# Performance work log

Hardware: AMD Instinct MI355X
Metric: run time of the kernel (lower is better)

Reference implementation:

```python
import jax, jax.numpy as jnp
import numpy as np

N_EMBD = 1024
N_HEAD = 16
HEAD_DIM = N_EMBD // N_HEAD
NEG = -1e9


def setup_inputs() -> dict:
    key = jax.random.key(0)
    ks = jax.random.split(key, 5)
    B, S = 2, 2048
    x = jax.random.normal(ks[0], (B, S, N_EMBD), dtype=jnp.float32)
    # qkv_proj: Linear(n_embd, 3*n_embd) -> weight used as x @ W_qkv (W stored [in, out])
    scale = 1.0 / np.sqrt(N_EMBD)
    W_qkv = jax.random.normal(ks[1], (N_EMBD, 3 * N_EMBD), dtype=jnp.float32) * scale
    b_qkv = jax.random.normal(ks[2], (3 * N_EMBD,), dtype=jnp.float32) * 0.02
    W_out = jax.random.normal(ks[3], (N_EMBD, N_EMBD), dtype=jnp.float32) * scale
    b_out = jax.random.normal(ks[4], (N_EMBD,), dtype=jnp.float32) * 0.02
    return {"x": x, "W_qkv": W_qkv, "b_qkv": b_qkv, "W_out": W_out, "b_out": b_out}


def reference(x, W_qkv, b_qkv, W_out, b_out):
    B, S, E = x.shape
    qkv = x @ W_qkv + b_qkv                      # [B,S,3E]
    q, k, v = jnp.split(qkv, 3, axis=-1)
    # [B,S,E] -> [B,H,S,D]
    def split_heads(t):
        return t.reshape(B, S, N_HEAD, HEAD_DIM).transpose(0, 2, 1, 3)
    q, k, v = split_heads(q), split_heads(k), split_heads(v)
    scores = jnp.einsum("bhqd,bhkd->bhqk", q, k) / jnp.sqrt(jnp.float32(HEAD_DIM))
    causal = jnp.tril(jnp.ones((S, S), dtype=bool))
    scores = jnp.where(causal, scores, NEG)
    attn = jax.nn.softmax(scores, axis=-1)
    out = jnp.einsum("bhqk,bhkd->bhqd", attn, v)  # [B,H,S,D]
    out = out.transpose(0, 2, 1, 3).reshape(B, S, E)
    return out @ W_out + b_out
```

## Files before the change

### kernel.cpp

```cpp
#include <hip/hip_runtime.h>
#include <hip/hip_bf16.h>

#define BATCH 2
#define SEQ   2048
#define EMBD  1024
#define NHEAD 16
#define HDIM  64
#define QKV3  (3 * EMBD)

#define QSCALE 0.18033688011112042f
#define SCLAMP 86.56f

typedef __attribute__((ext_vector_type(8))) __bf16 bf16x8;
typedef __attribute__((ext_vector_type(4))) __bf16 bf16x4;
typedef __attribute__((ext_vector_type(4))) float f32x4;

__device__ __forceinline__ float fast_exp2(float x) {
#if __has_builtin(__builtin_amdgcn_exp2f)
    return __builtin_amdgcn_exp2f(x);
#else
    return exp2f(x);
#endif
}

__global__ __launch_bounds__(256) void cast_f32_bf16(
    const float* __restrict__ in, __bf16* __restrict__ out)
{
    int i = (blockIdx.x * 256 + threadIdx.x) * 8;
    float4 a = *(const float4*)&in[i];
    float4 b = *(const float4*)&in[i + 4];
    bf16x8 o;
    o[0] = (__bf16)a.x; o[1] = (__bf16)a.y; o[2] = (__bf16)a.z; o[3] = (__bf16)a.w;
    o[4] = (__bf16)b.x; o[5] = (__bf16)b.y; o[6] = (__bf16)b.z; o[7] = (__bf16)b.w;
    *(bf16x8*)&out[i] = o;
}

__global__ __launch_bounds__(256) void transpose_cast_bf16(
    const float* __restrict__ in, __bf16* __restrict__ out, int K, int N)
{
    __shared__ float t[64][65];
    const int k0 = blockIdx.y * 64, n0 = blockIdx.x * 64;
    const int tid = threadIdx.x;
    #pragma unroll
    for (int p = 0; p < 4; p++) {
        int kr = p * 16 + (tid >> 4);
        int c4 = (tid & 15) * 4;
        float4 v = *(const float4*)&in[(size_t)(k0 + kr) * N + n0 + c4];
        t[kr][c4] = v.x; t[kr][c4 + 1] = v.y; t[kr][c4 + 2] = v.z; t[kr][c4 + 3] = v.w;
    }
    __syncthreads();
    #pragma unroll
    for (int p = 0; p < 4; p++) {
        int nr = p * 16 + (tid >> 4);
        int k4 = (tid & 15) * 4;
        bf16x4 o;
        o[0] = (__bf16)t[k4 + 0][nr];
        o[1] = (__bf16)t[k4 + 1][nr];
        o[2] = (__bf16)t[k4 + 2][nr];
        o[3] = (__bf16)t[k4 + 3][nr];
        *(bf16x4*)&out[(size_t)(n0 + nr) * K + k0 + k4] = o;
    }
}

__global__ __launch_bounds__(256) void transpose_v_bf16(
    const __bf16* __restrict__ qkv, __bf16* __restrict__ vt)
{
    __shared__ __bf16 t[64][72];
    const int k0 = blockIdx.x * 64;
    const int bh = blockIdx.y;
    const int b = bh >> 4, h = bh & 15;
    const size_t base = (size_t)b * SEQ * QKV3 + 2 * EMBD + h * HDIM;
    const int tid = threadIdx.x;
    #pragma unroll
    for (int it = 0; it < 2; it++) {
        int flat = it * 256 + tid;
        int kr = flat >> 3;
        int d0 = (flat & 7) * 8;
        bf16x8 v = *(const bf16x8*)&qkv[base + (size_t)(k0 + kr) * QKV3 + d0];
        #pragma unroll
        for (int i = 0; i < 8; i++) t[kr][d0 + i] = v[i];
    }
    __syncthreads();
    #pragma unroll
    for (int it = 0; it < 2; it++) {
        int flat = it * 256 + tid;
        int d  = flat >> 3;
        int kc = (flat & 7) * 8;
        bf16x8 o;
        #pragma unroll
        for (int i = 0; i < 8; i++) o[i] = t[kc + i][d];
        *(bf16x8*)&vt[((size_t)bh * 64 + d) * SEQ + k0 + kc] = o;
    }
}

template<bool OUT_BF16>
__global__ __launch_bounds__(256) void gemm_bt_mfma(
    const __bf16* __restrict__ A,
    const __bf16* __restrict__ Bt,
    const float* __restrict__ bias,
    void* __restrict__ Cv,
    int M, int N, int K, int nscale)
{
    __shared__ __align__(16) __bf16 As[128 * 32];
    __shared__ __align__(16) __bf16 Bs[128 * 32];

    const int tid  = threadIdx.x;
    const int lane = tid & 63;
    const int wave = tid >> 6;
    const int wm = (wave >> 1) * 64;
    const int wn = (wave & 1) * 64;
    const int m0 = blockIdx.y * 128;
    const int n0 = blockIdx.x * 128;
    const int lm = lane & 15;
    const int kq = lane >> 4;

    f32x4 acc[4][4] = {};

    for (int k0 = 0; k0 < K; k0 += 32) {
        __syncthreads();
        #pragma unroll
        for (int r = 0; r < 2; r++) {
            int flat = r * 256 + tid;
            int row  = flat >> 2;
            int off  = (flat & 3) * 16;
            const char* ga = (const char*)(A + (size_t)(m0 + row) * K + k0) + off;
            char* la = (char*)As + flat * 16;
            __builtin_amdgcn_global_load_lds(
                (const __attribute__((address_space(1))) void*)ga,
                (__attribute__((address_space(3))) void*)la, 16, 0, 0);
            const char* gb = (const char*)(Bt + (size_t)(n0 + row) * K + k0) + off;
            char* lb = (char*)Bs + flat * 16;
            __builtin_amdgcn_global_load_lds(
                (const __attribute__((address_space(1))) void*)gb,
                (__attribute__((address_space(3))) void*)lb, 16, 0, 0);
        }
        __syncthreads();

        bf16x8 af[4], bf[4];
        #pragma unroll
        for (int t = 0; t < 4; t++) {
            af[t] = *(const bf16x8*)&As[(wm + t * 16 + lm) * 32 + kq * 8];
            bf[t] = *(const bf16x8*)&Bs[(wn + t * 16 + lm) * 32 + kq * 8];
        }
        #pragma unroll
        for (int i = 0; i < 4; i++)
            #pragma unroll
            for (int j = 0; j < 4; j++)
                acc[i][j] = __builtin_amdgcn_mfma_f32_16x16x32_bf16(
                    af[i], bf[j], acc[i][j], 0, 0, 0);
    }

    const int r0 = kq * 4;
    #pragma unroll
    for (int i = 0; i < 4; i++) {
        #pragma unroll
        for (int j = 0; j < 4; j++) {
            int col = n0 + wn + j * 16 + lm;
            float bv = bias[col];
            float sc = (col < nscale) ? QSCALE : 1.0f;
            #pragma unroll
            for (int r = 0; r < 4; r++) {
                int row = m0 + wm + i * 16 + r0 + r;
                float val = (acc[i][j][r] + bv) * sc;
                if (OUT_BF16) ((__bf16*)Cv)[(size_t)row * N + col] = (__bf16)val;
                else          ((float*)Cv)[(size_t)row * N + col] = val;
            }
        }
    }
}

__global__ __launch_bounds__(256) void attn_kpar_mfma(
    const __bf16* __restrict__ qkv, const __bf16* __restrict__ vt,
    __bf16* __restrict__ attn)
{
    __shared__ __align__(16) char smem[34304];

    const int tid  = threadIdx.x;
    const int wave = tid >> 6;
    const int lane = tid & 63;
    const int quad = lane >> 4;
    const int c    = lane & 15;

    const int bh = blockIdx.x;
    const int b  = bh >> 4;
    const int h  = bh & 15;
    const int qblk = (int)(gridDim.y - 1) - blockIdx.y;
    const int q0 = qblk * 64;

    const size_t base = (size_t)b * SEQ * QKV3;
    const int hoff = h * HDIM;
    const __bf16* vbase = vt + (size_t)bh * 64 * SEQ;

    bf16x8 aq[4][2];
    #pragma unroll
    for (int qf = 0; qf < 4; qf++) {
        const __bf16* qrow = qkv + base +
            (size_t)(q0 + qf * 16 + c) * QKV3 + hoff + quad * 8;
        aq[qf][0] = *(const bf16x8*)(qrow);
        aq[qf][1] = *(const bf16x8*)(qrow + 32);
    }

    f32x4 acc[4][4] = {};
    float lpart[4] = {};

    char* pbw = smem + wave * 8192;
    const int ntiles = qblk + 1;

    for (int t = wave; t < ntiles; t += 4) {
        const int k0 = t * 64;
        const bool diag = (t == ntiles - 1);

        #pragma unroll
        for (int jj = 0; jj < 4; jj++) {
            const __bf16* krow = qkv + base +
                (size_t)(k0 + jj * 16 + c) * QKV3 + EMBD + hoff + quad * 8;
            bf16x8 bk0 = *(const bf16x8*)(krow);
            bf16x8 bk1 = *(const bf16x8*)(krow + 32);
            const int kb = k0 + jj * 16 + quad * 4;
            const int wb = (jj >> 1) * 1024 + (((jj & 1) * 2 + (quad >> 1))) * 256
                         + c * 16 + (quad & 1) * 8;
            #pragma unroll
            for (int qf = 0; qf < 4; qf++) {
                f32x4 s = {};
                s = __builtin_amdgcn_mfma_f32_16x16x32_bf16(bk0, aq[qf][0], s, 0, 0, 0);
                s = __builtin_amdgcn_mfma_f32_16x16x32_bf16(bk1, aq[qf][1], s, 0, 0, 0);
                const int qa = q0 + qf * 16 + c;
                bf16x4 pk;
                #pragma unroll
                for (int r = 0; r < 4; r++) {
                    float p;
                    if (diag && (kb + r > qa)) p = 0.f;
                    else p = fast_exp2(fminf(s[r], SCLAMP));
                    lpart[qf] += p;
                    pk[r] = (__bf16)p;
                }
                *(bf16x4*)(pbw + qf * 2048 + wb) = pk;
            }
        }

        __builtin_amdgcn_s_setprio(1);
        #pragma unroll
        for (int kc = 0; kc < 2; kc++) {
            bf16x8 ap[4];
            #pragma unroll
            for (int qf = 0; qf < 4; qf++)
                ap[qf] = *(const bf16x8*)(pbw + qf * 2048 + kc * 1024 + lane * 16);
            #pragma unroll
            for (int dd = 0; dd < 4; dd++) {
                const __bf16* vr = vbase + (size_t)(dd * 16 + c) * SEQ
                                 + k0 + kc * 32 + quad * 8;
                bf16x8 bv = *(const bf16x8*)(vr);
                #pragma unroll
                for (int qf = 0; qf < 4; qf++)
                    acc[qf][dd] = __builtin_amdgcn_mfma_f32_16x16x32_bf16(
                        ap[qf], bv, acc[qf][dd], 0, 0, 0);
            }
        }
        __builtin_amdgcn_s_setprio(0);
    }

    #pragma unroll
    for (int qf = 0; qf < 4; qf++) {
        float v = lpart[qf];
        v += __shfl_xor(v, 16);
        v += __shfl_xor(v, 32);
        lpart[qf] = v;
    }

    __syncthreads();

    float* Ored = (float*)smem;
    float* lred = (float*)(smem + 33792);

    if (wave < 2) {
        float* R = Ored + wave * (64 * 66);
        #pragma unroll
        for (int qf = 0; qf < 4; qf++) {
            #pragma unroll
            for (int dd = 0; dd < 4; dd++)
                #pragma unroll
                for (int r = 0; r < 4; r++)
                    R[(qf * 16 + quad * 4 + r) * 66 + dd * 16 + c] = acc[qf][dd][r];
            if (quad == 0) lred[wave * 64 + qf * 16 + c] = lpart[qf];
        }
    }
    __syncthreads();
    if (wave >= 2) {
        float* R = Ored + (wave - 2) * (64 * 66);
        #pragma unroll
        for (int qf = 0; qf < 4; qf++) {
            #pragma unroll
            for (int dd = 0; dd < 4; dd++)
                #pragma unroll
                for (int r = 0; r < 4; r++)
                    R[(qf * 16 + quad * 4 + r) * 66 + dd * 16 + c] += acc[qf][dd][r];
            if (quad == 0) lred[(wave - 2) * 64 + qf * 16 + c] += lpart[qf];
        }
    }
    __syncthreads();

    #pragma unroll
    for (int it = 0; it < 2; it++) {
        const int flat = it * 256 + tid;
        const int row = flat >> 3;
        const int cg  = flat & 7;
        const float l = lred[row] + lred[64 + row];
        const float inv = 1.f / l;
        const float* R0 = Ored + row * 66 + cg * 8;
        const float* R1 = R0 + 64 * 66;
        bf16x8 o;
        #pragma unroll
        for (int i = 0; i < 8; i++) o[i] = (__bf16)((R0[i] + R1[i]) * inv);
        *(bf16x8*)&attn[((size_t)b * SEQ + q0 + row) * EMBD + hoff + cg * 8] = o;
    }
}

extern "C" void kernel_launch(void* const* d_in, const int* in_sizes, int n_in,
                              void* d_out, int out_size, void* d_ws, size_t ws_size,
                              hipStream_t stream)
{
    const float* x     = (const float*)d_in[0];
    const float* W_qkv = (const float*)d_in[1];
    const float* b_qkv = (const float*)d_in[2];
    const float* W_out = (const float*)d_in[3];
    const float* b_out = (const float*)d_in[4];
    float* out = (float*)d_out;

    const int M = BATCH * SEQ;

    __bf16* xbf    = (__bf16*)d_ws;
    __bf16* Wqkv_t = xbf    + (size_t)M * EMBD;
    __bf16* Wout_t = Wqkv_t + (size_t)QKV3 * EMBD;
    __bf16* qkv    = Wout_t + (size_t)EMBD * EMBD;
    __bf16* attn   = qkv    + (size_t)M * QKV3;
    __bf16* vtbuf  = attn   + (size_t)M * EMBD;

    cast_f32_bf16<<<(M * EMBD) / (256 * 8), 256, 0, stream>>>(x, xbf);
    {
        dim3 g(QKV3 / 64, EMBD / 64);
        transpose_cast_bf16<<<g, 256, 0, stream>>>(W_qkv, Wqkv_t, EMBD, QKV3);
    }
    {
        dim3 g(EMBD / 64, EMBD / 64);
        transpose_cast_bf16<<<g, 256, 0, stream>>>(W_out, Wout_t, EMBD, EMBD);
    }
    {
        dim3 grid(QKV3 / 128, M / 128);
        gemm_bt_mfma<true><<<grid, 256, 0, stream>>>(xbf, Wqkv_t, b_qkv, qkv, M, QKV3, EMBD, EMBD);
    }
    {
        dim3 grid(SEQ / 64, BATCH * NHEAD);
        transpose_v_bf16<<<grid, 256, 0, stream>>>(qkv, vtbuf);
    }
    {
        dim3 grid(BATCH * NHEAD, SEQ / 64);
        attn_kpar_mfma<<<grid, 256, 0, stream>>>(qkv, vtbuf, attn);
    }
    {
        dim3 grid(EMBD / 128, M / 128);
        gemm_bt_mfma<false><<<grid, 256, 0, stream>>>(attn, Wout_t, b_out, out, M, EMBD, EMBD, 0);
    }
}
```

Baseline: 203.7 us.

## Prefetch K tiles into registers and remap blocks across XCDs

Each wave now loads the K tile for its next iteration into registers during the current iteration, and issues the V loads at the start of the tile so their latency overlaps the QK^T and softmax work. The block index is also remapped so consecutive hardware blocks, which are spread round-robin over the 8 XCDs, land on the same head's query blocks per XCD to improve L2 reuse of K/V. The change raises register pressure, which may lower occupancy, and the remap assumes a fixed grid of 1024 blocks.

```diff
diff --git a/kernel.cpp b/kernel.cpp
--- a/kernel.cpp
+++ b/kernel.cpp
@@ -181,10 +181,12 @@
     const int quad = lane >> 4;
     const int c    = lane & 15;
 
-    const int bh = blockIdx.x;
+    const int hw = (int)(blockIdx.x + gridDim.x * blockIdx.y);
+    const int logical = (hw & 7) * 128 + (hw >> 3);
+    const int bh   = logical >> 5;
+    const int qblk = 31 - (logical & 31);
     const int b  = bh >> 4;
     const int h  = bh & 15;
-    const int qblk = (int)(gridDim.y - 1) - blockIdx.y;
     const int q0 = qblk * 64;
 
     const size_t base = (size_t)b * SEQ * QKV3;
@@ -206,24 +208,40 @@
     char* pbw = smem + wave * 8192;
     const int ntiles = qblk + 1;
 
+    bf16x8 kreg[4][2];
+    {
+        const int k0p = wave * 64;
+        #pragma unroll
+        for (int jj = 0; jj < 4; jj++) {
+            const __bf16* krow = qkv + base +
+                (size_t)(k0p + jj * 16 + c) * QKV3 + EMBD + hoff + quad * 8;
+            kreg[jj][0] = *(const bf16x8*)(krow);
+            kreg[jj][1] = *(const bf16x8*)(krow + 32);
+        }
+    }
+
     for (int t = wave; t < ntiles; t += 4) {
         const int k0 = t * 64;
         const bool diag = (t == ntiles - 1);
 
+        bf16x8 vreg[2][4];
+        #pragma unroll
+        for (int kc = 0; kc < 2; kc++)
+            #pragma unroll
+            for (int dd = 0; dd < 4; dd++)
+                vreg[kc][dd] = *(const bf16x8*)(vbase
+                    + (size_t)(dd * 16 + c) * SEQ + k0 + kc * 32 + quad * 8);
+
         #pragma unroll
         for (int jj = 0; jj < 4; jj++) {
-            const __bf16* krow = qkv + base +
-                (size_t)(k0 + jj * 16 + c) * QKV3 + EMBD + hoff + quad * 8;
-            bf16x8 bk0 = *(const bf16x8*)(krow);
-            bf16x8 bk1 = *(const bf16x8*)(krow + 32);
             const int kb = k0 + jj * 16 + quad * 4;
             const int wb = (jj >> 1) * 1024 + (((jj & 1) * 2 + (quad >> 1))) * 256
                          + c * 16 + (quad & 1) * 8;
             #pragma unroll
             for (int qf = 0; qf < 4; qf++) {
                 f32x4 s = {};
-                s = __builtin_amdgcn_mfma_f32_16x16x32_bf16(bk0, aq[qf][0], s, 0, 0, 0);
-                s = __builtin_amdgcn_mfma_f32_16x16x32_bf16(bk1, aq[qf][1], s, 0, 0, 0);
+                s = __builtin_amdgcn_mfma_f32_16x16x32_bf16(kreg[jj][0], aq[qf][0], s, 0, 0, 0);
+                s = __builtin_amdgcn_mfma_f32_16x16x32_bf16(kreg[jj][1], aq[qf][1], s, 0, 0, 0);
                 const int qa = q0 + qf * 16 + c;
                 bf16x4 pk;
                 #pragma unroll
@@ -238,6 +256,17 @@
             }
         }
 
+        if (t + 4 < ntiles) {
+            const int k0n = k0 + 256;
+            #pragma unroll
+            for (int jj = 0; jj < 4; jj++) {
+                const __bf16* krow = qkv + base +
+                    (size_t)(k0n + jj * 16 + c) * QKV3 + EMBD + hoff + quad * 8;
+                kreg[jj][0] = *(const bf16x8*)(krow);
+                kreg[jj][1] = *(const bf16x8*)(krow + 32);
+            }
+        }
+
         __builtin_amdgcn_s_setprio(1);
         #pragma unroll
         for (int kc = 0; kc < 2; kc++) {
@@ -247,13 +276,10 @@
                 ap[qf] = *(const bf16x8*)(pbw + qf * 2048 + kc * 1024 + lane * 16);
             #pragma unroll
             for (int dd = 0; dd < 4; dd++) {
-                const __bf16* vr = vbase + (size_t)(dd * 16 + c) * SEQ
-                                 + k0 + kc * 32 + quad * 8;
-                bf16x8 bv = *(const bf16x8*)(vr);
                 #pragma unroll
                 for (int qf = 0; qf < 4; qf++)
                     acc[qf][dd] = __builtin_amdgcn_mfma_f32_16x16x32_bf16(
-                        ap[qf], bv, acc[qf][dd], 0, 0, 0);
+                        ap[qf], vreg[kc][dd], acc[qf][dd], 0, 0, 0);
             }
         }
         __builtin_amdgcn_s_setprio(0);
```

New measurement: 205.1 us. No clear change (+0.7%).

## Switch attention to 32x32 MFMA with in-register P via permlane32 swap

Applied to the files above, without the earlier changes.

Rewrites the attention inner loop to use 32x32x16 bf16 MFMAs instead of 16x16x32, and converts the softmax probabilities into the A-operand layout in registers with v_cvt_pk_bf16 and v_permlane32_swap. This removes the per-wave LDS round trip for P and its associated shared-memory stores and loads. K and V fragments for a whole tile are now preloaded into registers up front, which raises register pressure and may reduce occupancy. The pre-reduction __syncthreads is also dropped because P no longer lives in shared memory.

```diff
diff --git a/kernel.cpp b/kernel.cpp
--- a/kernel.cpp
+++ b/kernel.cpp
@@ -11,9 +11,11 @@
 #define QSCALE 0.18033688011112042f
 #define SCLAMP 86.56f
 
-typedef __attribute__((ext_vector_type(8))) __bf16 bf16x8;
-typedef __attribute__((ext_vector_type(4))) __bf16 bf16x4;
-typedef __attribute__((ext_vector_type(4))) float f32x4;
+typedef __attribute__((ext_vector_type(8)))  __bf16 bf16x8;
+typedef __attribute__((ext_vector_type(4)))  __bf16 bf16x4;
+typedef __attribute__((ext_vector_type(4)))  float  f32x4;
+typedef __attribute__((ext_vector_type(16))) float  f32x16;
+typedef __attribute__((ext_vector_type(4)))  unsigned int u32x4;
 
 __device__ __forceinline__ float fast_exp2(float x) {
 #if __has_builtin(__builtin_amdgcn_exp2f)
@@ -21,6 +23,21 @@
 #else
     return exp2f(x);
 #endif
+}
+
+__device__ __forceinline__ unsigned pk_bf16(float a, float b) {
+    unsigned d;
+    asm("v_cvt_pk_bf16_f32 %0, %1, %2" : "=v"(d) : "v"(a), "v"(b));
+    return d;
+}
+
+__device__ __forceinline__ void pl32_swap(unsigned &a, unsigned &b) {
+    asm volatile("v_permlane32_swap_b32 %0, %1" : "+v"(a), "+v"(b));
+}
+
+__device__ __forceinline__ bf16x8 frag4(unsigned a, unsigned b, unsigned c, unsigned d) {
+    u32x4 u = {a, b, c, d};
+    return __builtin_bit_cast(bf16x8, u);
 }
 
 __global__ __launch_bounds__(256) void cast_f32_bf16(
@@ -178,8 +195,10 @@
     const int tid  = threadIdx.x;
     const int wave = tid >> 6;
     const int lane = tid & 63;
-    const int quad = lane >> 4;
-    const int c    = lane & 15;
+    const int l31  = lane & 31;
+    const int hi   = lane >> 5;
+    const int hi4  = hi * 4;
+    const int hi8  = hi * 8;
 
     const int bh = blockIdx.x;
     const int b  = bh >> 4;
@@ -191,83 +210,102 @@
     const int hoff = h * HDIM;
     const __bf16* vbase = vt + (size_t)bh * 64 * SEQ;
 
-    bf16x8 aq[4][2];
-    #pragma unroll
-    for (int qf = 0; qf < 4; qf++) {
+    bf16x8 aq[2][4];
+    #pragma unroll
+    for (int qh = 0; qh < 2; qh++) {
         const __bf16* qrow = qkv + base +
-            (size_t)(q0 + qf * 16 + c) * QKV3 + hoff + quad * 8;
-        aq[qf][0] = *(const bf16x8*)(qrow);
-        aq[qf][1] = *(const bf16x8*)(qrow + 32);
-    }
-
-    f32x4 acc[4][4] = {};
-    float lpart[4] = {};
-
-    char* pbw = smem + wave * 8192;
+            (size_t)(q0 + qh * 32 + l31) * QKV3 + hoff + hi8;
+        #pragma unroll
+        for (int ds = 0; ds < 4; ds++)
+            aq[qh][ds] = *(const bf16x8*)(qrow + ds * 16);
+    }
+
+    f32x16 acc[2][2] = {};
+    float lpart[2] = {};
+
     const int ntiles = qblk + 1;
 
     for (int t = wave; t < ntiles; t += 4) {
         const int k0 = t * 64;
         const bool diag = (t == ntiles - 1);
 
-        #pragma unroll
-        for (int jj = 0; jj < 4; jj++) {
+        bf16x8 kf[2][4];
+        #pragma unroll
+        for (int kh = 0; kh < 2; kh++) {
             const __bf16* krow = qkv + base +
-                (size_t)(k0 + jj * 16 + c) * QKV3 + EMBD + hoff + quad * 8;
-            bf16x8 bk0 = *(const bf16x8*)(krow);
-            bf16x8 bk1 = *(const bf16x8*)(krow + 32);
-            const int kb = k0 + jj * 16 + quad * 4;
-            const int wb = (jj >> 1) * 1024 + (((jj & 1) * 2 + (quad >> 1))) * 256
-                         + c * 16 + (quad & 1) * 8;
-            #pragma unroll
-            for (int qf = 0; qf < 4; qf++) {
-                f32x4 s = {};
-                s = __builtin_amdgcn_mfma_f32_16x16x32_bf16(bk0, aq[qf][0], s, 0, 0, 0);
-                s = __builtin_amdgcn_mfma_f32_16x16x32_bf16(bk1, aq[qf][1], s, 0, 0, 0);
-                const int qa = q0 + qf * 16 + c;
-                bf16x4 pk;
+                (size_t)(k0 + kh * 32 + l31) * QKV3 + EMBD + hoff + hi8;
+            #pragma unroll
+            for (int ds = 0; ds < 4; ds++)
+                kf[kh][ds] = *(const bf16x8*)(krow + ds * 16);
+        }
+        bf16x8 vf[2][2][2];
+        #pragma unroll
+        for (int kh = 0; kh < 2; kh++)
+            #pragma unroll
+            for (int ks = 0; ks < 2; ks++)
                 #pragma unroll
-                for (int r = 0; r < 4; r++) {
-                    float p;
-                    if (diag && (kb + r > qa)) p = 0.f;
-                    else p = fast_exp2(fminf(s[r], SCLAMP));
-                    lpart[qf] += p;
-                    pk[r] = (__bf16)p;
+                for (int dh = 0; dh < 2; dh++)
+                    vf[kh][ks][dh] = *(const bf16x8*)(vbase
+                        + (size_t)(dh * 32 + l31) * SEQ
+                        + k0 + kh * 32 + ks * 16 + hi8);
+
+        #pragma unroll
+        for (int kh = 0; kh < 2; kh++) {
+            #pragma unroll
+            for (int qh = 0; qh < 2; qh++) {
+                f32x16 s = {};
+                #pragma unroll
+                for (int ds = 0; ds < 4; ds++)
+                    s = __builtin_amdgcn_mfma_f32_32x32x16_bf16(
+                        kf[kh][ds], aq[qh][ds], s, 0, 0, 0);
+
+                float p[16];
+                const int qa = q0 + qh * 32 + l31;
+                if (diag) {
+                    const int kb = k0 + kh * 32 + hi4;
+                    #pragma unroll
+                    for (int r = 0; r < 16; r++) {
+                        const int ka = kb + (r & 3) + 8 * (r >> 2);
+                        float v = fast_exp2(fminf(s[r], SCLAMP));
+                        p[r] = (ka > qa) ? 0.f : v;
+                        lpart[qh] += p[r];
+                    }
+                } else {
+                    #pragma unroll
+                    for (int r = 0; r < 16; r++) {
+                        p[r] = fast_exp2(fminf(s[r], SCLAMP));
+                        lpart[qh] += p[r];
+                    }
                 }
-                *(bf16x4*)(pbw + qf * 2048 + wb) = pk;
+
+                unsigned X0 = pk_bf16(p[0],  p[1]),  X1 = pk_bf16(p[2],  p[3]);
+                unsigned Y0 = pk_bf16(p[4],  p[5]),  Y1 = pk_bf16(p[6],  p[7]);
+                unsigned Z0 = pk_bf16(p[8],  p[9]),  Z1 = pk_bf16(p[10], p[11]);
+                unsigned W0 = pk_bf16(p[12], p[13]), W1 = pk_bf16(p[14], p[15]);
+                pl32_swap(X0, Y0); pl32_swap(X1, Y1);
+                pl32_swap(Z0, W0); pl32_swap(Z1, W1);
+                bf16x8 pa0 = frag4(X0, X1, Y0, Y1);
+                bf16x8 pa1 = frag4(Z0, Z1, W0, W1);
+
+                __builtin_amdgcn_s_setprio(1);
+                #pragma unroll
+                for (int dh = 0; dh < 2; dh++) {
+                    acc[qh][dh] = __builtin_amdgcn_mfma_f32_32x32x16_bf16(
+                        pa0, vf[kh][0][dh], acc[qh][dh], 0, 0, 0);
+                    acc[qh][dh] = __builtin_amdgcn_mfma_f32_32x32x16_bf16(
+                        pa1, vf[kh][1][dh], acc[qh][dh], 0, 0, 0);
+                }
+                __builtin_amdgcn_s_setprio(0);
             }
         }
-
-        __builtin_amdgcn_s_setprio(1);
-        #pragma unroll
-        for (int kc = 0; kc < 2; kc++) {
-            bf16x8 ap[4];
-            #pragma unroll
-            for (int qf = 0; qf < 4; qf++)
-                ap[qf] = *(const bf16x8*)(pbw + qf * 2048 + kc * 1024 + lane * 16);
-            #pragma unroll
-            for (int dd = 0; dd < 4; dd++) {
-                const __bf16* vr = vbase + (size_t)(dd * 16 + c) * SEQ
-                                 + k0 + kc * 32 + quad * 8;
-                bf16x8 bv = *(const bf16x8*)(vr);
-                #pragma unroll
-                for (int qf = 0; qf < 4; qf++)
-                    acc[qf][dd] = __builtin_amdgcn_mfma_f32_16x16x32_bf16(
-                        ap[qf], bv, acc[qf][dd], 0, 0, 0);
-            }
-        }
-        __builtin_amdgcn_s_setprio(0);
-    }
-
-    #pragma unroll
-    for (int qf = 0; qf < 4; qf++) {
-        float v = lpart[qf];
-        v += __shfl_xor(v, 16);
+    }
+
+    #pragma unroll
+    for (int qh = 0; qh < 2; qh++) {
+        float v = lpart[qh];
         v += __shfl_xor(v, 32);
-        lpart[qf] = v;
-    }
-
-    __syncthreads();
+        lpart[qh] = v;
+    }
 
     float* Ored = (float*)smem;
     float* lred = (float*)(smem + 33792);
@@ -275,26 +313,28 @@
     if (wave < 2) {
         float* R = Ored + wave * (64 * 66);
         #pragma unroll
-        for (int qf = 0; qf < 4; qf++) {
-            #pragma unroll
-            for (int dd = 0; dd < 4; dd++)
+        for (int qh = 0; qh < 2; qh++) {
+            #pragma unroll
+            for (int dh = 0; dh < 2; dh++)
                 #pragma unroll
-                for (int r = 0; r < 4; r++)
-                    R[(qf * 16 + quad * 4 + r) * 66 + dd * 16 + c] = acc[qf][dd][r];
-            if (quad == 0) lred[wave * 64 + qf * 16 + c] = lpart[qf];
+                for (int r = 0; r < 16; r++)
+                    R[(qh * 32 + (r & 3) + 8 * (r >> 2) + hi4) * 66
+                      + dh * 32 + l31] = acc[qh][dh][r];
+            if (hi == 0) lred[wave * 64 + qh * 32 + l31] = lpart[qh];
         }
     }
     __syncthreads();
     if (wave >= 2) {
         float* R = Ored + (wave - 2) * (64 * 66);
         #pragma unroll
-        for (int qf = 0; qf < 4; qf++) {
-            #pragma unroll
-            for (int dd = 0; dd < 4; dd++)
+        for (int qh = 0; qh < 2; qh++) {
+            #pragma unroll
+            for (int dh = 0; dh < 2; dh++)
                 #pragma unroll
-                for (int r = 0; r < 4; r++)
-                    R[(qf * 16 + quad * 4 + r) * 66 + dd * 16 + c] += acc[qf][dd][r];
-            if (quad == 0) lred[(wave - 2) * 64 + qf * 16 + c] += lpart[qf];
+                for (int r = 0; r < 16; r++)
+                    R[(qh * 32 + (r & 3) + 8 * (r >> 2) + hi4) * 66
+                      + dh * 32 + l31] += acc[qh][dh][r];
+            if (hi == 0) lred[(wave - 2) * 64 + qh * 32 + l31] += lpart[qh];
         }
     }
     __syncthreads();
```

Result: no change. 204.2 us (+0.2%).
